# Kernel optimization log

Hardware: AMD Instinct MI355X
Metric: run time of the kernel (lower is better)

Reference implementation:

```python
import jax, jax.numpy as jnp
import numpy as np
import math

B, L = 16, 100
NC = 80
STRIDES = (8.0, 16.0, 32.0)
ANCHORS = np.array([[10., 13.], [16., 30.], [33., 23.], [30., 61.], [62., 45.],
                    [59., 119.], [116., 90.], [156., 198.], [373., 326.]], np.float32)
ANCH_MASKS = ((0, 1, 2), (3, 4, 5), (6, 7, 8))
THRESH = 4.0          # gt_match_max_ratio
CIOU_RATIO = 1.0
W_BOX, W_OBJ, W_CLS = 0.05, 1.0, 0.58
OV = 0.5              # overlap in assign_targets_to_proposals


def _bce(x, z):
    # binary_cross_entropy_with_logits, elementwise
    return -(z * jax.nn.log_sigmoid(x) + (1.0 - z) * jax.nn.log_sigmoid(-x))


def _ciou_xywh(b1, b2, eps=1e-9):
    # b1, b2: [M,4] center-x, center-y, w, h  (matches _bbox_iou with x1y1x2y2=False, CIoU=True)
    b1x1, b1x2 = b1[:, 0] - b1[:, 2] / 2, b1[:, 0] + b1[:, 2] / 2
    b1y1, b1y2 = b1[:, 1] - b1[:, 3] / 2, b1[:, 1] + b1[:, 3] / 2
    b2x1, b2x2 = b2[:, 0] - b2[:, 2] / 2, b2[:, 0] + b2[:, 2] / 2
    b2y1, b2y2 = b2[:, 1] - b2[:, 3] / 2, b2[:, 1] + b2[:, 3] / 2
    inter = jnp.clip(jnp.minimum(b1x2, b2x2) - jnp.maximum(b1x1, b2x1), 0) * \
            jnp.clip(jnp.minimum(b1y2, b2y2) - jnp.maximum(b1y1, b2y1), 0)
    w1, h1 = b1x2 - b1x1, b1y2 - b1y1 + eps
    w2, h2 = b2x2 - b2x1, b2y2 - b2y1 + eps
    union = w1 * h1 + w2 * h2 - inter + eps
    iou = inter / union
    cw = jnp.maximum(b1x2, b2x2) - jnp.minimum(b1x1, b2x1)
    ch = jnp.maximum(b1y2, b2y2) - jnp.minimum(b1y1, b2y1)
    c2 = cw ** 2 + ch ** 2 + eps
    rho2 = ((b2x1 + b2x2 - b1x1 - b1x2) ** 2 + (b2y1 + b2y2 - b1y1 - b1y2) ** 2) / 4
    v = (4.0 / math.pi ** 2) * (jnp.arctan(w2 / h2) - jnp.arctan(w1 / h1)) ** 2
    alpha = jax.lax.stop_gradient(v / (1.0 + eps - iou + v))  # torch.no_grad()
    return iou - (rho2 / c2 + v * alpha)


def _yolo_loss(y_pred0, y_pred1, y_pred2, y_true):
    # valid GT rows: nlabel counts rows with positive sum; valid rows assumed contiguous at front
    nlabel = (y_true.sum(-1) > 0).sum(-1)                                # [B]
    valid = (jnp.arange(L)[None, :] < nlabel[:, None]).reshape(-1)       # [N]
    batch_ids = jnp.repeat(jnp.arange(B), L)                             # [N]
    flat = y_true.reshape(-1, 5)
    gt_labels = flat[:, 4].astype(jnp.int32)
    # convert x1,y1,w,h -> cx,cy,w,h
    gt_boxes = jnp.concatenate([flat[:, :2] + flat[:, 2:4] / 2, flat[:, 2:4]], axis=1)
    N = B * L
    offsets = jnp.array([[0, 0], [-OV, 0], [0, -OV], [OV, 0], [0, OV]], jnp.float32)
    loss_box = jnp.float32(0.0)
    loss_obj = jnp.float32(0.0)
    loss_cls = jnp.float32(0.0)
    for li, out in enumerate((y_pred0, y_pred1, y_pred2)):
        s = STRIDES[li]
        anch = jnp.asarray(ANCHORS[list(ANCH_MASKS[li])] / s)            # [3,2] grid units
        H, Wd = out.shape[2], out.shape[3]
        nch = 5 + NC
        p = out.reshape(B, -1, nch, H, Wd).transpose(0, 1, 3, 4, 2)      # [B,3,H,W,nch]
        sgb = gt_boxes / s                                               # [N,4]
        # size_matched_idx
        r = sgb[:, None, 2:4] / anch[None]                               # [N,3,2]
        maxr = jnp.maximum(r, 1.0 / r).max(-1)                           # [N,3]
        match = (maxr < THRESH) & valid[:, None]                         # [N,3]
        # assign_targets_to_proposals: 5 offset candidates per (gt, anchor)
        x, y = sgb[:, 0], sgb[:, 1]
        fx, fy = jnp.mod(x, 1.0), jnp.mod(y, 1.0)
        cond = jnp.stack([
            jnp.ones_like(x, bool),
            (x > 1) & (fx < OV),
            (y > 1) & (fy < OV),
            (x < Wd - 1) & (fx > 1 - OV),
            (y < H - 1) & (fy > 1 - OV),
        ], axis=1)                                                       # [N,5]
        coords = (sgb[:, None, :2] + offsets[None]).astype(jnp.int32)    # [N,5,2] (trunc like .long())
        cmask = (match[:, :, None] & cond[:, None, :]).reshape(-1)       # [N*3*5]
        bf = jnp.broadcast_to(batch_ids[:, None, None], (N, 3, 5)).reshape(-1)
        af = jnp.broadcast_to(jnp.arange(3)[None, :, None], (N, 3, 5)).reshape(-1)
        gf = jnp.broadcast_to(jnp.arange(N)[:, None, None], (N, 3, 5)).reshape(-1)
        gxy = jnp.broadcast_to(coords[:, None, :, :], (N, 3, 5, 2)).reshape(-1, 2)
        gx, gy = gxy[:, 0], gxy[:, 1]
        pred = p[bf, af, gy, gx]                                         # [M,nch] (OOB gathers clamped; masked out)
        pxy = jax.nn.sigmoid(pred[:, :2]) + gxy.astype(pred.dtype)
        pwh = jnp.exp(pred[:, 2:4]) * anch[af]
        pbox = jnp.concatenate([pxy, pwh], axis=1)
        ci = _ciou_xywh(pbox, sgb[gf])                                   # [M]
        cm = cmask.astype(pred.dtype)
        nval = cm.sum()
        denom = jnp.maximum(nval, 1.0)
        loss_box = loss_box + jnp.where(nval > 0, ((1.0 - ci) * cm).sum() / denom, 0.0)
        # objectness target scatter (invalid candidates dropped via OOB batch index)
        obj_val = CIOU_RATIO * jnp.clip(ci, 0) + (1.0 - CIOU_RATIO)
        bs = jnp.where(cmask, bf, B)
        gt_obj = jnp.zeros((B, 3, H, Wd), pred.dtype).at[bs, af, gy, gx].set(obj_val, mode='drop')
        if NC > 1:
            zhot = jax.nn.one_hot(gt_labels[gf], NC, dtype=pred.dtype)
            bce_c = _bce(pred[:, 5:], zhot)
            loss_cls = loss_cls + jnp.where(nval > 0, (bce_c * cm[:, None]).sum() / (denom * NC), 0.0)
        loss_obj = loss_obj + _bce(p[..., 4], gt_obj).mean()
    lb, lo, lc = W_BOX * loss_box, W_OBJ * loss_obj, W_CLS * loss_cls
    return lb + lo + lc, lb, lo, lc


def setup_inputs():
    rng = np.random.default_rng(0)
    k0, k1, k2 = jax.random.split(jax.random.key(0), 3)
    y_pred0 = jax.random.normal(k0, (B, 3 * (5 + NC), 80, 80), jnp.float32)
    y_pred1 = jax.random.normal(k1, (B, 3 * (5 + NC), 40, 40), jnp.float32)
    y_pred2 = jax.random.normal(k2, (B, 3 * (5 + NC), 20, 20), jnp.float32)
    yt = np.zeros((B, L, 5), np.float32)
    n_valid = 70  # valid labels contiguous at the front, rest zero-padded
    yt[:, :n_valid, 0] = rng.uniform(1.0, 560.0, (B, n_valid))
    yt[:, :n_valid, 1] = rng.uniform(1.0, 560.0, (B, n_valid))
    yt[:, :n_valid, 2] = rng.uniform(8.0, 80.0, (B, n_valid))
    yt[:, :n_valid, 3] = rng.uniform(8.0, 80.0, (B, n_valid))
    yt[:, :n_valid, 4] = rng.integers(0, NC, (B, n_valid)).astype(np.float32)
    return {"y_pred0": y_pred0, "y_pred1": y_pred1, "y_pred2": y_pred2, "y_true": jnp.asarray(yt)}


def reference(y_pred0, y_pred1, y_pred2, y_true):
    return _yolo_loss(y_pred0, y_pred1, y_pred2, y_true)
```

## Files before the change

kernel.cpp:

```cpp
#include <hip/hip_runtime.h>
#include <math.h>

#define BB 16
#define LL 100
#define NCLS 80
#define CPB 282
#define CAP 288
#define PREPB 256
#define GATB 4608
#define OBJB 99
#define NTHR 1024

__device__ __constant__ int   d_W[3]     = {80, 40, 20};
__device__ __constant__ int   d_HW[3]    = {6400, 1600, 400};
__device__ __constant__ float d_stride[3]= {8.f, 16.f, 32.f};
__device__ __constant__ int   d_gtoff[3] = {0, 307200, 384000};
__device__ __constant__ float d_anch[3][3][2] = {
  {{10.f,13.f},{16.f,30.f},{33.f,23.f}},
  {{30.f,61.f},{62.f,45.f},{59.f,119.f}},
  {{116.f,90.f},{156.f,198.f},{373.f,326.f}}};

#define ACC_OFF   0
#define CNT_OFF   16
#define CANDG_OFF 272

__device__ __forceinline__ float softplusf(float t) {
  return fmaxf(t, 0.f) + log1pf(expf(-fabsf(t)));
}
__device__ __forceinline__ float sigmoidf_(float x) {
  return 1.f / (1.f + expf(-x));
}

__device__ __forceinline__ float ciou_(float px, float py, float pw, float ph,
                                       float gx, float gy, float gw, float gh) {
  const float eps = 1e-9f;
  float b1x1 = px - pw*0.5f, b1x2 = px + pw*0.5f;
  float b1y1 = py - ph*0.5f, b1y2 = py + ph*0.5f;
  float b2x1 = gx - gw*0.5f, b2x2 = gx + gw*0.5f;
  float b2y1 = gy - gh*0.5f, b2y2 = gy + gh*0.5f;
  float iw = fmaxf(fminf(b1x2,b2x2) - fmaxf(b1x1,b2x1), 0.f);
  float ih = fmaxf(fminf(b1y2,b2y2) - fmaxf(b1y1,b2y1), 0.f);
  float inter = iw*ih;
  float w1 = b1x2-b1x1, h1 = b1y2-b1y1 + eps;
  float w2 = b2x2-b2x1, h2 = b2y2-b2y1 + eps;
  float uni = w1*h1 + w2*h2 - inter + eps;
  float iou = inter/uni;
  float cw = fmaxf(b1x2,b2x2) - fminf(b1x1,b2x1);
  float ch = fmaxf(b1y2,b2y2) - fminf(b1y1,b2y1);
  float c2 = cw*cw + ch*ch + eps;
  float dx = b2x1+b2x2-b1x1-b1x2;
  float dy = b2y1+b2y2-b1y1-b1y2;
  float rho2 = (dx*dx + dy*dy)*0.25f;
  float at = atanf(w2/h2) - atanf(w1/h1);
  float v = (float)(4.0/(M_PI*M_PI)) * at*at;
  float alpha = v / (1.0f + eps - iou + v);
  return iou - (rho2/c2 + v*alpha);
}

__global__ __launch_bounds__(512)
void k_prep(const float* __restrict__ yt, float* __restrict__ acc,
            unsigned int* __restrict__ cntg, unsigned int* __restrict__ candg)
{
  __shared__ int s_nl[2];
  __shared__ int s_cnt;
  const int blk = blockIdx.x, tid = threadIdx.x;

  if (blk == 0 && tid >= 32 && tid < 48) acc[tid-32] = 0.f;

  if (tid < 2)  s_nl[tid] = 0;
  if (tid == 2) s_cnt = 0;

  const int t0 = blk*CPB;
  const int b_lo = t0/4500;
  int b_hi = (t0 + CPB - 1)/4500; if (b_hi > BB-1) b_hi = BB-1;
  __syncthreads();

  if (tid < LL) {
    const float* row = yt + (size_t)(b_lo*LL + tid)*5;
    if (row[0]+row[1]+row[2]+row[3]+row[4] > 0.f) atomicAdd(&s_nl[0], 1);
  } else if (tid >= 128 && tid < 128+LL && b_hi != b_lo) {
    const float* row = yt + (size_t)(b_hi*LL + (tid-128))*5;
    if (row[0]+row[1]+row[2]+row[3]+row[4] > 0.f) atomicAdd(&s_nl[1], 1);
  }
  __syncthreads();

  if (tid < CPB) {
    int t = t0 + tid;
    if (t < BB*LL*45) {
      int b = t/4500; int rem = t - b*4500;
      int g_loc = rem/45; int rem2 = rem - g_loc*45;
      int lvl = rem2/15, ao = rem2 - lvl*15, a = ao/5, o = ao - a*5;
      const float* row = yt + (size_t)(b*LL + g_loc)*5;
      float s = d_stride[lvl];
      int W = d_W[lvl];
      float cx = (row[0] + row[2]*0.5f)/s;
      float cy = (row[1] + row[3]*0.5f)/s;
      float w = row[2]/s, h = row[3]/s;
      float aw = d_anch[lvl][a][0]/s, ah = d_anch[lvl][a][1]/s;
      float rw = w/aw, rh = h/ah;
      float maxr = fmaxf(fmaxf(rw,1.f/rw), fmaxf(rh,1.f/rh));
      int nl = (b == b_lo) ? s_nl[0] : s_nl[1];
      bool m = (g_loc < nl) && (maxr < 4.0f);
      float fx = cx - floorf(cx), fy = cy - floorf(cy);
      bool c;
      switch (o) {
        case 0: c = true; break;
        case 1: c = (cx > 1.f) && (fx < 0.5f); break;
        case 2: c = (cy > 1.f) && (fy < 0.5f); break;
        case 3: c = (cx < (float)(W-1)) && (fx > 0.5f); break;
        default:c = (cy < (float)(W-1)) && (fy > 0.5f); break;
      }
      if (m && c) {
        const float offx[5] = {0.f,-0.5f,0.f,0.5f,0.f};
        const float offy[5] = {0.f,0.f,-0.5f,0.f,0.5f};
        int gx = (int)(cx + offx[o]);
        int gy = (int)(cy + offy[o]);
        int g = b*LL + g_loc;
        unsigned pk = ((unsigned)lvl<<27) | ((unsigned)a<<25) | ((unsigned)g<<14)
                    | ((unsigned)gy<<7) | (unsigned)gx;
        int idx = atomicAdd(&s_cnt, 1);
        candg[blk*CAP + idx] = pk;
      }
    }
  }
  __syncthreads();
  if (tid == 0) cntg[blk] = (unsigned)s_cnt;
}

__global__ __launch_bounds__(NTHR)
void k_gather(const float* __restrict__ p0, const float* __restrict__ p1,
              const float* __restrict__ p2, const float* __restrict__ yt,
              const unsigned int* __restrict__ cntg,
              const unsigned int* __restrict__ candg,
              float* __restrict__ acc)
{
  __shared__ float s_acc[15];
  const int blk = blockIdx.x, tid = threadIdx.x;
  if (tid < 15) s_acc[tid] = 0.f;
  __syncthreads();

  if (blk < GATB) {
    int wg = blk*16 + (tid >> 6);
    int lane = tid & 63;
    int p = wg / CAP;
    int sIdx = wg - p*CAP;
    if (sIdx < (int)cntg[p]) {
      unsigned pk = candg[p*CAP + sIdx];
      int gx  = pk & 127;
      int gy  = (pk>>7) & 127;
      int g   = (pk>>14) & 2047;
      int a   = (pk>>25) & 3;
      int lvl = (pk>>27) & 3;
      int b = g / LL;
      float s = d_stride[lvl];
      int W = d_W[lvl], HW = d_HW[lvl];
      const float* pr = (lvl==0) ? p0 : (lvl==1) ? p1 : p2;
      const float* row = yt + (size_t)g*5;
      float cx = (row[0] + row[2]*0.5f)/s;
      float cy = (row[1] + row[3]*0.5f)/s;
      float w  = row[2]/s, h = row[3]/s;
      int label = (int)row[4];
      float aw = d_anch[lvl][a][0]/s, ah = d_anch[lvl][a][1]/s;

      const float* base = pr + (size_t)((b*255 + a*85)*HW + gy*W + gx);
      float xA = base[(size_t)lane*HW];
      float xB = (lane < 21) ? base[(size_t)(64+lane)*HW] : 0.f;
      float x0 = __shfl(xA,0), x1 = __shfl(xA,1), x2 = __shfl(xA,2), x3 = __shfl(xA,3);
      float xobj = __shfl(xA,4);

      float pxc = sigmoidf_(x0) + (float)gx;
      float pyc = sigmoidf_(x1) + (float)gy;
      float pw = expf(x2)*aw, ph = expf(x3)*ah;
      float ci = ciou_(pxc,pyc,pw,ph, cx,cy,w,h);

      float cls = 0.f;
      if (lane >= 5) { int cc = lane-5;  cls += (cc==label) ? softplusf(-xA) : softplusf(xA); }
      if (lane < 21) { int cc = 59+lane; cls += (cc==label) ? softplusf(-xB) : softplusf(xB); }
      for (int off = 1; off < 64; off <<= 1) cls += __shfl_xor(cls, off);

      if (lane == 0) {
        float bx = 1.f - ci;
        float zx = fmaxf(ci, 0.f) * xobj;
        atomicAdd(&s_acc[lvl],     bx);
        atomicAdd(&s_acc[3+lvl],  cls);
        atomicAdd(&s_acc[6+lvl],  1.f);
        atomicAdd(&s_acc[12+lvl], zx);
      }
    }
  } else {
    int gt = (blk - GATB)*NTHR + tid;
    if (gt < 100800) {
      int e0 = gt*4;
      int lvl = (e0 < 307200) ? 0 : (e0 < 384000 ? 1 : 2);
      int HW = d_HW[lvl];
      int idx = e0 - d_gtoff[lvl];
      int b = idx/(3*HW); int r2 = idx - b*3*HW; int a = r2/HW; int pos = r2 - a*HW;
      const float* pr = (lvl==0) ? p0 : (lvl==1) ? p1 : p2;
      const float4 x4 = *(const float4*)(pr + (size_t)((b*255 + a*85 + 4)*HW + pos));
      float sp = softplusf(x4.x) + softplusf(x4.y) + softplusf(x4.z) + softplusf(x4.w);
      atomicAdd(&s_acc[9+lvl], sp);
    }
  }
  __syncthreads();
  if (tid < 15 && s_acc[tid] != 0.f) atomicAdd(&acc[tid], s_acc[tid]);
}

__global__ __launch_bounds__(64)
void k_fin(const float* __restrict__ acc, float* __restrict__ out) {
  if (threadIdx.x != 0) return;
  const float cells[3] = {307200.f, 76800.f, 19200.f};
  float lb = 0.f, lc = 0.f, lo = 0.f;
  for (int l = 0; l < 3; ++l) {
    float nval  = acc[6+l];
    float denom = fmaxf(nval, 1.f);
    if (nval > 0.f) {
      lb += acc[l] / denom;
      lc += acc[3+l] / (denom * (float)NCLS);
    }
    lo += (acc[9+l] - acc[12+l]) / cells[l];
  }
  lb *= 0.05f;
  lc *= 0.58f;
  out[0] = lb + lo + lc;
  out[1] = lb;
  out[2] = lo;
  out[3] = lc;
}

extern "C" void kernel_launch(void* const* d_in, const int* in_sizes, int n_in,
                              void* d_out, int out_size, void* d_ws, size_t ws_size,
                              hipStream_t stream) {
  const float* p0 = (const float*)d_in[0];
  const float* p1 = (const float*)d_in[1];
  const float* p2 = (const float*)d_in[2];
  const float* yt = (const float*)d_in[3];

  float*        wsf   = (float*)d_ws;
  float*        acc   = wsf + ACC_OFF;
  unsigned int* cntg  = (unsigned int*)(wsf + CNT_OFF);
  unsigned int* candg = (unsigned int*)(wsf + CANDG_OFF);

  k_prep  <<<PREPB, 512, 0, stream>>>(yt, acc, cntg, candg);
  k_gather<<<GATB + OBJB, NTHR, 0, stream>>>(p0, p1, p2, yt, cntg, candg, acc);
  k_fin   <<<1, 64, 0, stream>>>(acc, (float*)d_out);
}
```

Before: 47.71 us.

## Precompute dense per-cell class softplus sums, then scatter candidates via single-thread lookups

Replaces the per-candidate 64-lane gather of all 85 channels with two stages. A dense pass sums softplus over the 80 class channels for every anchor cell, writes the sums to a workspace buffer, and also accumulates the objectness softplus. A scatter kernel then handles each candidate with one thread: it reads only the box and objectness channels plus the single label logit, and gets the class loss as the cell sum minus the label logit, using softplus(-x) = softplus(x) - x. This removes scattered strided gathers and the launch of thousands of mostly idle 1024-thread blocks, at the cost of streaming all class channels of every cell rather than only matched cells.

```diff
diff --git a/kernel.cpp b/kernel.cpp
--- a/kernel.cpp
+++ b/kernel.cpp
@@ -7,9 +7,6 @@
 #define CPB 282
 #define CAP 288
 #define PREPB 256
-#define GATB 4608
-#define OBJB 99
-#define NTHR 1024
 
 __device__ __constant__ int   d_W[3]     = {80, 40, 20};
 __device__ __constant__ int   d_HW[3]    = {6400, 1600, 400};
@@ -23,6 +20,7 @@
 #define ACC_OFF   0
 #define CNT_OFF   16
 #define CANDG_OFF 272
+#define S_OFF     74000
 
 __device__ __forceinline__ float softplusf(float t) {
   return fmaxf(t, 0.f) + log1pf(expf(-fabsf(t)));
@@ -127,82 +125,111 @@
   if (tid == 0) cntg[blk] = (unsigned)s_cnt;
 }
 
-__global__ __launch_bounds__(NTHR)
-void k_gather(const float* __restrict__ p0, const float* __restrict__ p1,
-              const float* __restrict__ p2, const float* __restrict__ yt,
-              const unsigned int* __restrict__ cntg,
-              const unsigned int* __restrict__ candg,
-              float* __restrict__ acc)
+__global__ __launch_bounds__(256)
+void k_cellsum(const float* __restrict__ p0, const float* __restrict__ p1,
+               const float* __restrict__ p2, float* __restrict__ S,
+               float* __restrict__ acc)
 {
-  __shared__ float s_acc[15];
-  const int blk = blockIdx.x, tid = threadIdx.x;
-  if (tid < 15) s_acc[tid] = 0.f;
-  __syncthreads();
-
-  if (blk < GATB) {
-    int wg = blk*16 + (tid >> 6);
-    int lane = tid & 63;
-    int p = wg / CAP;
-    int sIdx = wg - p*CAP;
-    if (sIdx < (int)cntg[p]) {
-      unsigned pk = candg[p*CAP + sIdx];
-      int gx  = pk & 127;
-      int gy  = (pk>>7) & 127;
-      int g   = (pk>>14) & 2047;
-      int a   = (pk>>25) & 3;
-      int lvl = (pk>>27) & 3;
-      int b = g / LL;
-      float s = d_stride[lvl];
-      int W = d_W[lvl], HW = d_HW[lvl];
-      const float* pr = (lvl==0) ? p0 : (lvl==1) ? p1 : p2;
-      const float* row = yt + (size_t)g*5;
-      float cx = (row[0] + row[2]*0.5f)/s;
-      float cy = (row[1] + row[3]*0.5f)/s;
-      float w  = row[2]/s, h = row[3]/s;
-      int label = (int)row[4];
-      float aw = d_anch[lvl][a][0]/s, ah = d_anch[lvl][a][1]/s;
-
-      const float* base = pr + (size_t)((b*255 + a*85)*HW + gy*W + gx);
-      float xA = base[(size_t)lane*HW];
-      float xB = (lane < 21) ? base[(size_t)(64+lane)*HW] : 0.f;
-      float x0 = __shfl(xA,0), x1 = __shfl(xA,1), x2 = __shfl(xA,2), x3 = __shfl(xA,3);
-      float xobj = __shfl(xA,4);
-
-      float pxc = sigmoidf_(x0) + (float)gx;
-      float pyc = sigmoidf_(x1) + (float)gy;
-      float pw = expf(x2)*aw, ph = expf(x3)*ah;
-      float ci = ciou_(pxc,pyc,pw,ph, cx,cy,w,h);
-
-      float cls = 0.f;
-      if (lane >= 5) { int cc = lane-5;  cls += (cc==label) ? softplusf(-xA) : softplusf(xA); }
-      if (lane < 21) { int cc = 59+lane; cls += (cc==label) ? softplusf(-xB) : softplusf(xB); }
-      for (int off = 1; off < 64; off <<= 1) cls += __shfl_xor(cls, off);
-
-      if (lane == 0) {
-        float bx = 1.f - ci;
-        float zx = fmaxf(ci, 0.f) * xobj;
-        atomicAdd(&s_acc[lvl],     bx);
-        atomicAdd(&s_acc[3+lvl],  cls);
-        atomicAdd(&s_acc[6+lvl],  1.f);
-        atomicAdd(&s_acc[12+lvl], zx);
-      }
+  __shared__ float s_obj[3];
+  const int tid = threadIdx.x;
+  if (tid < 3) s_obj[tid] = 0.f;
+  __syncthreads();
+
+  int gt = blockIdx.x*256 + tid;
+  bool act = gt < 100800;
+  float so = 0.f;
+  int lvl = 0, e0 = 0;
+  const float* cbase = nullptr;
+  size_t HW = 0;
+
+  if (act) {
+    e0 = gt*4;
+    lvl = (e0 < 307200) ? 0 : (e0 < 384000 ? 1 : 2);
+    int HWi = d_HW[lvl];
+    int idx = e0 - d_gtoff[lvl];
+    int b = idx/(3*HWi); int r2 = idx - b*3*HWi; int a = r2/HWi; int pos = r2 - a*HWi;
+    const float* pr = (lvl==0) ? p0 : (lvl==1) ? p1 : p2;
+    cbase = pr + (size_t)((b*255 + a*85)*HWi + pos);
+    HW = (size_t)HWi;
+    const float4 o4 = *(const float4*)(cbase + 4*HW);
+    so = softplusf(o4.x) + softplusf(o4.y) + softplusf(o4.z) + softplusf(o4.w);
+  }
+  for (int off = 1; off < 64; off <<= 1) so += __shfl_xor(so, off);
+  if ((tid & 63) == 0 && so != 0.f) atomicAdd(&s_obj[lvl], so);
+
+  if (act) {
+    float4 s4 = make_float4(0.f, 0.f, 0.f, 0.f);
+    #pragma unroll 10
+    for (int c = 0; c < 80; ++c) {
+      const float4 x4 = *(const float4*)(cbase + (size_t)(5+c)*HW);
+      s4.x += softplusf(x4.x); s4.y += softplusf(x4.y);
+      s4.z += softplusf(x4.z); s4.w += softplusf(x4.w);
     }
-  } else {
-    int gt = (blk - GATB)*NTHR + tid;
-    if (gt < 100800) {
-      int e0 = gt*4;
-      int lvl = (e0 < 307200) ? 0 : (e0 < 384000 ? 1 : 2);
-      int HW = d_HW[lvl];
-      int idx = e0 - d_gtoff[lvl];
-      int b = idx/(3*HW); int r2 = idx - b*3*HW; int a = r2/HW; int pos = r2 - a*HW;
-      const float* pr = (lvl==0) ? p0 : (lvl==1) ? p1 : p2;
-      const float4 x4 = *(const float4*)(pr + (size_t)((b*255 + a*85 + 4)*HW + pos));
-      float sp = softplusf(x4.x) + softplusf(x4.y) + softplusf(x4.z) + softplusf(x4.w);
-      atomicAdd(&s_acc[9+lvl], sp);
-    }
-  }
-  __syncthreads();
-  if (tid < 15 && s_acc[tid] != 0.f) atomicAdd(&acc[tid], s_acc[tid]);
+    *(float4*)(S + e0) = s4;
+  }
+  __syncthreads();
+  if (tid < 3 && s_obj[tid] != 0.f) atomicAdd(&acc[9+tid], s_obj[tid]);
+}
+
+__global__ __launch_bounds__(256)
+void k_scatter(const float* __restrict__ p0, const float* __restrict__ p1,
+               const float* __restrict__ p2, const float* __restrict__ yt,
+               const float* __restrict__ S,
+               const unsigned int* __restrict__ cntg,
+               const unsigned int* __restrict__ candg,
+               float* __restrict__ acc)
+{
+  __shared__ float s_acc[12];
+  const int tid = threadIdx.x;
+  if (tid < 12) s_acc[tid] = 0.f;
+  __syncthreads();
+
+  int slot = blockIdx.x*256 + tid;
+  int p = slot / CAP;
+  int sIdx = slot - p*CAP;
+  if (sIdx < (int)cntg[p]) {
+    unsigned pk = candg[p*CAP + sIdx];
+    int gx  = pk & 127;
+    int gy  = (pk>>7) & 127;
+    int g   = (pk>>14) & 2047;
+    int a   = (pk>>25) & 3;
+    int lvl = (pk>>27) & 3;
+    int b = g / LL;
+    float s = d_stride[lvl];
+    int W = d_W[lvl], HW = d_HW[lvl];
+    const float* pr = (lvl==0) ? p0 : (lvl==1) ? p1 : p2;
+    const float* row = yt + (size_t)g*5;
+    float cx = (row[0] + row[2]*0.5f)/s;
+    float cy = (row[1] + row[3]*0.5f)/s;
+    float w  = row[2]/s, h = row[3]/s;
+    int label = (int)row[4];
+    float aw = d_anch[lvl][a][0]/s, ah = d_anch[lvl][a][1]/s;
+
+    int cell = (b*3 + a)*HW + gy*W + gx;
+    const float* base = pr + (size_t)(b*255 + a*85)*HW + (size_t)(gy*W + gx);
+    float x0 = base[0];
+    float x1 = base[(size_t)HW];
+    float x2 = base[2*(size_t)HW];
+    float x3 = base[3*(size_t)HW];
+    float x4 = base[4*(size_t)HW];
+    float xl = base[(size_t)(5+label)*HW];
+    float Sc = S[d_gtoff[lvl] + cell];
+
+    float pxc = sigmoidf_(x0) + (float)gx;
+    float pyc = sigmoidf_(x1) + (float)gy;
+    float pw = expf(x2)*aw, ph = expf(x3)*ah;
+    float ci = ciou_(pxc,pyc,pw,ph, cx,cy,w,h);
+
+    atomicAdd(&s_acc[lvl],     1.f - ci);
+    atomicAdd(&s_acc[3+lvl],   Sc - xl);
+    atomicAdd(&s_acc[6+lvl],   1.f);
+    atomicAdd(&s_acc[9+lvl],   fmaxf(ci, 0.f) * x4);
+  }
+  __syncthreads();
+  if (tid < 12 && s_acc[tid] != 0.f) {
+    int dst = (tid < 9) ? tid : (tid + 3);
+    atomicAdd(&acc[dst], s_acc[tid]);
+  }
 }
 
 __global__ __launch_bounds__(64)
@@ -239,8 +266,10 @@
   float*        acc   = wsf + ACC_OFF;
   unsigned int* cntg  = (unsigned int*)(wsf + CNT_OFF);
   unsigned int* candg = (unsigned int*)(wsf + CANDG_OFF);
-
-  k_prep  <<<PREPB, 512, 0, stream>>>(yt, acc, cntg, candg);
-  k_gather<<<GATB + OBJB, NTHR, 0, stream>>>(p0, p1, p2, yt, cntg, candg, acc);
-  k_fin   <<<1, 64, 0, stream>>>(acc, (float*)d_out);
-}
+  float*        S     = wsf + S_OFF;
+
+  k_prep   <<<PREPB, 512, 0, stream>>>(yt, acc, cntg, candg);
+  k_cellsum<<<(100800 + 255)/256, 256, 0, stream>>>(p0, p1, p2, S, acc);
+  k_scatter<<<73728/256, 256, 0, stream>>>(p0, p1, p2, yt, S, cntg, candg, acc);
+  k_fin    <<<1, 64, 0, stream>>>(acc, (float*)d_out);
+}
```

Result: slower. 151.3 us (+217.1%).

## Compact candidates globally and move objectness softplus sum into prep kernel

Applied to the files above, without the earlier changes.

Candidate anchors are now compacted into one dense global list, using a wave ballot plus one global atomic per wave, in place of fixed per-block slots. The gather kernel runs a grid-stride loop over only the real candidates instead of launching 4608 mostly idle blocks. The objectness softplus reduction moves into the prep kernel, reduced with wave shuffles, and a memset clears the accumulators. This trades an extra memset call and global atomics for far fewer launched waves.

```diff
diff --git a/kernel.cpp b/kernel.cpp
--- a/kernel.cpp
+++ b/kernel.cpp
@@ -5,11 +5,9 @@
 #define LL 100
 #define NCLS 80
 #define CPB 282
-#define CAP 288
 #define PREPB 256
-#define GATB 4608
-#define OBJB 99
-#define NTHR 1024
+#define GATB 1152
+#define GATW (GATB*16)
 
 __device__ __constant__ int   d_W[3]     = {80, 40, 20};
 __device__ __constant__ int   d_HW[3]    = {6400, 1600, 400};
@@ -21,8 +19,8 @@
   {{116.f,90.f},{156.f,198.f},{373.f,326.f}}};
 
 #define ACC_OFF   0
-#define CNT_OFF   16
-#define CANDG_OFF 272
+#define NCAND_OFF 16
+#define CAND_OFF  32
 
 __device__ __forceinline__ float softplusf(float t) {
   return fmaxf(t, 0.f) + log1pf(expf(-fabsf(t)));
@@ -58,17 +56,17 @@
 }
 
 __global__ __launch_bounds__(512)
-void k_prep(const float* __restrict__ yt, float* __restrict__ acc,
-            unsigned int* __restrict__ cntg, unsigned int* __restrict__ candg)
+void k_prep(const float* __restrict__ p0, const float* __restrict__ p1,
+            const float* __restrict__ p2, const float* __restrict__ yt,
+            float* __restrict__ acc, unsigned int* __restrict__ ncand,
+            unsigned int* __restrict__ candg)
 {
   __shared__ int s_nl[2];
-  __shared__ int s_cnt;
+  __shared__ float s_obj[3];
   const int blk = blockIdx.x, tid = threadIdx.x;
 
-  if (blk == 0 && tid >= 32 && tid < 48) acc[tid-32] = 0.f;
-
-  if (tid < 2)  s_nl[tid] = 0;
-  if (tid == 2) s_cnt = 0;
+  if (tid < 2) s_nl[tid] = 0;
+  if (tid >= 4 && tid < 7) s_obj[tid-4] = 0.f;
 
   const int t0 = blk*CPB;
   const int b_lo = t0/4500;
@@ -84,53 +82,86 @@
   }
   __syncthreads();
 
-  if (tid < CPB) {
-    int t = t0 + tid;
-    if (t < BB*LL*45) {
-      int b = t/4500; int rem = t - b*4500;
-      int g_loc = rem/45; int rem2 = rem - g_loc*45;
-      int lvl = rem2/15, ao = rem2 - lvl*15, a = ao/5, o = ao - a*5;
-      const float* row = yt + (size_t)(b*LL + g_loc)*5;
-      float s = d_stride[lvl];
-      int W = d_W[lvl];
-      float cx = (row[0] + row[2]*0.5f)/s;
-      float cy = (row[1] + row[3]*0.5f)/s;
-      float w = row[2]/s, h = row[3]/s;
-      float aw = d_anch[lvl][a][0]/s, ah = d_anch[lvl][a][1]/s;
-      float rw = w/aw, rh = h/ah;
-      float maxr = fmaxf(fmaxf(rw,1.f/rw), fmaxf(rh,1.f/rh));
-      int nl = (b == b_lo) ? s_nl[0] : s_nl[1];
-      bool m = (g_loc < nl) && (maxr < 4.0f);
-      float fx = cx - floorf(cx), fy = cy - floorf(cy);
-      bool c;
-      switch (o) {
-        case 0: c = true; break;
-        case 1: c = (cx > 1.f) && (fx < 0.5f); break;
-        case 2: c = (cy > 1.f) && (fy < 0.5f); break;
-        case 3: c = (cx < (float)(W-1)) && (fx > 0.5f); break;
-        default:c = (cy < (float)(W-1)) && (fy > 0.5f); break;
+  {
+    int gt = blk*512 + tid;
+    float so = 0.f; int lvl = 0;
+    if (gt < 100800) {
+      int e0 = gt*4;
+      lvl = (e0 < 307200) ? 0 : (e0 < 384000 ? 1 : 2);
+      int HW = d_HW[lvl];
+      int idx = e0 - d_gtoff[lvl];
+      int b = idx/(3*HW); int r2 = idx - b*3*HW; int a = r2/HW; int pos = r2 - a*HW;
+      const float* pr = (lvl==0) ? p0 : (lvl==1) ? p1 : p2;
+      const float4 o4 = *(const float4*)(pr + (size_t)((b*255 + a*85 + 4)*HW + pos));
+      so = softplusf(o4.x) + softplusf(o4.y) + softplusf(o4.z) + softplusf(o4.w);
+    }
+    for (int off = 1; off < 64; off <<= 1) so += __shfl_xor(so, off);
+    if ((tid & 63) == 0 && so != 0.f) atomicAdd(&s_obj[lvl], so);
+  }
+
+  {
+    bool act = false; unsigned pk = 0;
+    if (tid < CPB) {
+      int t = t0 + tid;
+      if (t < BB*LL*45) {
+        int b = t/4500; int rem = t - b*4500;
+        int g_loc = rem/45; int rem2 = rem - g_loc*45;
+        int lvl = rem2/15, ao = rem2 - lvl*15, a = ao/5, o = ao - a*5;
+        const float* row = yt + (size_t)(b*LL + g_loc)*5;
+        float s = d_stride[lvl];
+        int W = d_W[lvl];
+        float cx = (row[0] + row[2]*0.5f)/s;
+        float cy = (row[1] + row[3]*0.5f)/s;
+        float w = row[2]/s, h = row[3]/s;
+        float aw = d_anch[lvl][a][0]/s, ah = d_anch[lvl][a][1]/s;
+        float rw = w/aw, rh = h/ah;
+        float maxr = fmaxf(fmaxf(rw,1.f/rw), fmaxf(rh,1.f/rh));
+        int nl = (b == b_lo) ? s_nl[0] : s_nl[1];
+        bool m = (g_loc < nl) && (maxr < 4.0f);
+        float fx = cx - floorf(cx), fy = cy - floorf(cy);
+        bool c;
+        switch (o) {
+          case 0: c = true; break;
+          case 1: c = (cx > 1.f) && (fx < 0.5f); break;
+          case 2: c = (cy > 1.f) && (fy < 0.5f); break;
+          case 3: c = (cx < (float)(W-1)) && (fx > 0.5f); break;
+          default:c = (cy < (float)(W-1)) && (fy > 0.5f); break;
+        }
+        if (m && c) {
+          const float offx[5] = {0.f,-0.5f,0.f,0.5f,0.f};
+          const float offy[5] = {0.f,0.f,-0.5f,0.f,0.5f};
+          int gx = (int)(cx + offx[o]);
+          int gy = (int)(cy + offy[o]);
+          int g = b*LL + g_loc;
+          pk = ((unsigned)lvl<<27) | ((unsigned)a<<25) | ((unsigned)g<<14)
+             | ((unsigned)gy<<7) | (unsigned)gx;
+          act = true;
+        }
       }
-      if (m && c) {
-        const float offx[5] = {0.f,-0.5f,0.f,0.5f,0.f};
-        const float offy[5] = {0.f,0.f,-0.5f,0.f,0.5f};
-        int gx = (int)(cx + offx[o]);
-        int gy = (int)(cy + offy[o]);
-        int g = b*LL + g_loc;
-        unsigned pk = ((unsigned)lvl<<27) | ((unsigned)a<<25) | ((unsigned)g<<14)
-                    | ((unsigned)gy<<7) | (unsigned)gx;
-        int idx = atomicAdd(&s_cnt, 1);
-        candg[blk*CAP + idx] = pk;
+    }
+    unsigned long long mball = __ballot(act);
+    int cnt = __popcll(mball);
+    if (cnt) {
+      int lane = tid & 63;
+      int leader = __ffsll((unsigned long long)mball) - 1;
+      int base = 0;
+      if (lane == leader) base = (int)atomicAdd(ncand, (unsigned)cnt);
+      base = __shfl(base, leader);
+      if (act) {
+        int pre = __popcll(mball & ((1ULL<<lane)-1ULL));
+        candg[base + pre] = pk;
       }
     }
   }
-  __syncthreads();
-  if (tid == 0) cntg[blk] = (unsigned)s_cnt;
-}
-
-__global__ __launch_bounds__(NTHR)
+
+  __syncthreads();
+  if (tid < 3 && s_obj[tid] != 0.f) atomicAdd(&acc[9+tid], s_obj[tid]);
+}
+
+__global__ __launch_bounds__(1024)
 void k_gather(const float* __restrict__ p0, const float* __restrict__ p1,
               const float* __restrict__ p2, const float* __restrict__ yt,
-              const unsigned int* __restrict__ cntg,
+              const unsigned int* __restrict__ ncand,
               const unsigned int* __restrict__ candg,
               float* __restrict__ acc)
 {
@@ -139,66 +170,51 @@
   if (tid < 15) s_acc[tid] = 0.f;
   __syncthreads();
 
-  if (blk < GATB) {
-    int wg = blk*16 + (tid >> 6);
-    int lane = tid & 63;
-    int p = wg / CAP;
-    int sIdx = wg - p*CAP;
-    if (sIdx < (int)cntg[p]) {
-      unsigned pk = candg[p*CAP + sIdx];
-      int gx  = pk & 127;
-      int gy  = (pk>>7) & 127;
-      int g   = (pk>>14) & 2047;
-      int a   = (pk>>25) & 3;
-      int lvl = (pk>>27) & 3;
-      int b = g / LL;
-      float s = d_stride[lvl];
-      int W = d_W[lvl], HW = d_HW[lvl];
-      const float* pr = (lvl==0) ? p0 : (lvl==1) ? p1 : p2;
-      const float* row = yt + (size_t)g*5;
-      float cx = (row[0] + row[2]*0.5f)/s;
-      float cy = (row[1] + row[3]*0.5f)/s;
-      float w  = row[2]/s, h = row[3]/s;
-      int label = (int)row[4];
-      float aw = d_anch[lvl][a][0]/s, ah = d_anch[lvl][a][1]/s;
-
-      const float* base = pr + (size_t)((b*255 + a*85)*HW + gy*W + gx);
-      float xA = base[(size_t)lane*HW];
-      float xB = (lane < 21) ? base[(size_t)(64+lane)*HW] : 0.f;
-      float x0 = __shfl(xA,0), x1 = __shfl(xA,1), x2 = __shfl(xA,2), x3 = __shfl(xA,3);
-      float xobj = __shfl(xA,4);
-
-      float pxc = sigmoidf_(x0) + (float)gx;
-      float pyc = sigmoidf_(x1) + (float)gy;
-      float pw = expf(x2)*aw, ph = expf(x3)*ah;
-      float ci = ciou_(pxc,pyc,pw,ph, cx,cy,w,h);
-
-      float cls = 0.f;
-      if (lane >= 5) { int cc = lane-5;  cls += (cc==label) ? softplusf(-xA) : softplusf(xA); }
-      if (lane < 21) { int cc = 59+lane; cls += (cc==label) ? softplusf(-xB) : softplusf(xB); }
-      for (int off = 1; off < 64; off <<= 1) cls += __shfl_xor(cls, off);
-
-      if (lane == 0) {
-        float bx = 1.f - ci;
-        float zx = fmaxf(ci, 0.f) * xobj;
-        atomicAdd(&s_acc[lvl],     bx);
-        atomicAdd(&s_acc[3+lvl],  cls);
-        atomicAdd(&s_acc[6+lvl],  1.f);
-        atomicAdd(&s_acc[12+lvl], zx);
-      }
-    }
-  } else {
-    int gt = (blk - GATB)*NTHR + tid;
-    if (gt < 100800) {
-      int e0 = gt*4;
-      int lvl = (e0 < 307200) ? 0 : (e0 < 384000 ? 1 : 2);
-      int HW = d_HW[lvl];
-      int idx = e0 - d_gtoff[lvl];
-      int b = idx/(3*HW); int r2 = idx - b*3*HW; int a = r2/HW; int pos = r2 - a*HW;
-      const float* pr = (lvl==0) ? p0 : (lvl==1) ? p1 : p2;
-      const float4 x4 = *(const float4*)(pr + (size_t)((b*255 + a*85 + 4)*HW + pos));
-      float sp = softplusf(x4.x) + softplusf(x4.y) + softplusf(x4.z) + softplusf(x4.w);
-      atomicAdd(&s_acc[9+lvl], sp);
+  const int nc = (int)*ncand;
+  const int wv = blk*16 + (tid >> 6);
+  const int lane = tid & 63;
+
+  for (int i = wv; i < nc; i += GATW) {
+    unsigned pk = candg[i];
+    int gx  = pk & 127;
+    int gy  = (pk>>7) & 127;
+    int g   = (pk>>14) & 2047;
+    int a   = (pk>>25) & 3;
+    int lvl = (pk>>27) & 3;
+    int b = g / LL;
+    float s = d_stride[lvl];
+    int W = d_W[lvl], HW = d_HW[lvl];
+    const float* pr = (lvl==0) ? p0 : (lvl==1) ? p1 : p2;
+    const float* row = yt + (size_t)g*5;
+    float cx = (row[0] + row[2]*0.5f)/s;
+    float cy = (row[1] + row[3]*0.5f)/s;
+    float w  = row[2]/s, h = row[3]/s;
+    int label = (int)row[4];
+    float aw = d_anch[lvl][a][0]/s, ah = d_anch[lvl][a][1]/s;
+
+    const float* base = pr + (size_t)((b*255 + a*85)*HW + gy*W + gx);
+    float xA = base[(size_t)lane*HW];
+    float xB = (lane < 21) ? base[(size_t)(64+lane)*HW] : 0.f;
+    float x0 = __shfl(xA,0), x1 = __shfl(xA,1), x2 = __shfl(xA,2), x3 = __shfl(xA,3);
+    float xobj = __shfl(xA,4);
+
+    float pxc = sigmoidf_(x0) + (float)gx;
+    float pyc = sigmoidf_(x1) + (float)gy;
+    float pw = expf(x2)*aw, ph = expf(x3)*ah;
+    float ci = ciou_(pxc,pyc,pw,ph, cx,cy,w,h);
+
+    float cls = 0.f;
+    if (lane >= 5) { int cc = lane-5;  cls += (cc==label) ? softplusf(-xA) : softplusf(xA); }
+    if (lane < 21) { int cc = 59+lane; cls += (cc==label) ? softplusf(-xB) : softplusf(xB); }
+    for (int off = 1; off < 64; off <<= 1) cls += __shfl_xor(cls, off);
+
+    if (lane == 0) {
+      float bx = 1.f - ci;
+      float zx = fmaxf(ci, 0.f) * xobj;
+      atomicAdd(&s_acc[lvl],     bx);
+      atomicAdd(&s_acc[3+lvl],  cls);
+      atomicAdd(&s_acc[6+lvl],  1.f);
+      atomicAdd(&s_acc[12+lvl], zx);
     }
   }
   __syncthreads();
@@ -237,10 +253,11 @@
 
   float*        wsf   = (float*)d_ws;
   float*        acc   = wsf + ACC_OFF;
-  unsigned int* cntg  = (unsigned int*)(wsf + CNT_OFF);
-  unsigned int* candg = (unsigned int*)(wsf + CANDG_OFF);
-
-  k_prep  <<<PREPB, 512, 0, stream>>>(yt, acc, cntg, candg);
-  k_gather<<<GATB + OBJB, NTHR, 0, stream>>>(p0, p1, p2, yt, cntg, candg, acc);
+  unsigned int* ncand = (unsigned int*)(wsf + NCAND_OFF);
+  unsigned int* candg = (unsigned int*)(wsf + CAND_OFF);
+
+  hipMemsetAsync(d_ws, 0, 128, stream);
+  k_prep  <<<PREPB, 512, 0, stream>>>(p0, p1, p2, yt, acc, ncand, candg);
+  k_gather<<<GATB, 1024, 0, stream>>>(p0, p1, p2, yt, ncand, candg, acc);
   k_fin   <<<1, 64, 0, stream>>>(acc, (float*)d_out);
 }
```

New measurement: 57.11 us. 19.7% more time.
